# Kernel optimization log

Hardware: AMD Instinct MI355X
Metric: run time of the kernel (lower is better)

The kernel has to match this reference:

```python
import jax, jax.numpy as jnp
import numpy as np

B, N, M, C = 64, 16384, 64, 256
GAMMA = 0.95
EPS = 1e-16


def setup_inputs() -> dict:
    key = jax.random.key(0)
    k0, k1, k2, k3, k4 = jax.random.split(key, 5)
    embeddings = jax.random.normal(k0, (B, C), jnp.float32)
    # previous (w_u, w_r, w_lu) state; normalize so rows look like attention weights
    w_prev = jax.nn.softmax(jax.random.normal(k1, (B, 3, N), jnp.float32), axis=-1)
    memory = jax.random.normal(k2, (B, N, M), jnp.float32) * 0.05
    # fc_write params: xavier_uniform(gain=1.4) weight, N(0, 0.01) bias
    fan_in, fan_out = C, M + 2
    bound = 1.4 * np.sqrt(6.0 / (fan_in + fan_out))
    W = jax.random.uniform(k3, (M + 2, C), jnp.float32, -bound, bound)
    b = jax.random.normal(k4, (M + 2,), jnp.float32) * 0.01
    return {"embeddings": embeddings, "w_prev": w_prev, "memory": memory,
            "W": W, "b": b, "n": 4}


def reference(embeddings, w_prev, memory, W, b, n):
    # fc_write: [B,C] -> [B, M+2], split into key k, strength beta, gate g
    o = embeddings @ W.T + b
    k = o[:, :M]                                   # [B, M]
    beta = jax.nn.softplus(o[:, M:M + 1])          # [B, 1]
    g = jax.nn.sigmoid(o[:, M + 1:M + 2])          # [B, 1]

    w_u_prev = w_prev[:, 0]                        # usage
    w_r_prev = w_prev[:, 1]                        # read
    w_lu_prev = w_prev[:, 2]                       # least-used

    # content addressing: cosine similarity of k against every memory slot
    sim = jnp.einsum('bm,bnm->bn', k, memory) / (
        jnp.linalg.norm(k, axis=-1, keepdims=True)
        * jnp.linalg.norm(memory, axis=-1) + EPS)   # [B, N]
    w_r = jax.nn.softmax(beta * sim, axis=-1)       # [B, N]

    # LRUA write weight: interpolate previous read and least-used weights
    w_w = g * w_r_prev + (1.0 - g) * w_lu_prev      # [B, N]
    # usage decay + accumulate
    w_u = GAMMA * w_u_prev + w_r + w_w              # [B, N]

    # least-used: 1 at the n smallest-usage slots, 0 elsewhere
    _, lu_idx = jax.lax.top_k(-w_u, n)              # [B, n]
    w_lu = jnp.zeros_like(w_u).at[
        jnp.arange(w_u.shape[0])[:, None], lu_idx].set(1.0)

    # lrua_write: rank-1 additive write into memory
    new_memory = memory + w_w[:, :, None] * k[:, None, :]  # [B, N, M]

    w = jnp.stack([w_u, w_r, w_lu], axis=1)         # [B, 3, N]
    return w, new_memory
```

## Files before the change

kernel.cpp:

```cpp
#include <hip/hip_runtime.h>
#include <math.h>

#define Bn 64
#define Nn 16384
#define Mn 64
#define Cn 256
#define MP2 66
#define GAMMA 0.95f
#define EPSF 1e-16f

__global__ __launch_bounds__(128) void k1_proj(
    const float* __restrict__ emb, const float* __restrict__ W,
    const float* __restrict__ bias,
    float* __restrict__ ws_k, float* __restrict__ ws_beta,
    float* __restrict__ ws_g, float* __restrict__ ws_normk) {
  int b = blockIdx.x;
  int tid = threadIdx.x;
  __shared__ float emb_s[Cn];
  __shared__ float k_s[Mn];
  for (int c = tid; c < Cn; c += blockDim.x) emb_s[c] = emb[(size_t)b * Cn + c];
  __syncthreads();
  if (tid < MP2) {
    float sum = bias[tid];
    const float* wrow = W + (size_t)tid * Cn;
    #pragma unroll 4
    for (int c = 0; c < Cn; ++c) sum += emb_s[c] * wrow[c];
    if (tid < Mn) {
      ws_k[(size_t)b * Mn + tid] = sum;
      k_s[tid] = sum;
    } else if (tid == Mn) {
      ws_beta[b] = fmaxf(sum, 0.0f) + log1pf(expf(-fabsf(sum)));
    } else {
      ws_g[b] = 1.0f / (1.0f + expf(-sum));
    }
  }
  __syncthreads();
  if (tid < 64) {
    float v = k_s[tid] * k_s[tid];
    #pragma unroll
    for (int o = 32; o > 0; o >>= 1) v += __shfl_xor(v, o, 64);
    if (tid == 0) ws_normk[b] = sqrtf(v);
  }
}

__global__ __launch_bounds__(256) void k2_main(
    const float* __restrict__ memory, const float* __restrict__ w_prev,
    const float* __restrict__ ws_k, const float* __restrict__ ws_g,
    const float* __restrict__ ws_normk, const float* __restrict__ ws_beta,
    float* __restrict__ p_out, float* __restrict__ new_mem) {
  const int ROWS_PER_BLOCK = 16;
  const int blocks_per_b = Nn / ROWS_PER_BLOCK;
  int b = blockIdx.x / blocks_per_b;
  int n_base = (blockIdx.x % blocks_per_b) * ROWS_PER_BLOCK;
  int tid = threadIdx.x;
  int wave = tid >> 6;
  int lane = tid & 63;
  int row_in_wave = lane >> 4;
  int col4 = lane & 15;
  int n = n_base + wave * 4 + row_in_wave;

  size_t off = ((size_t)b * Nn + n) * Mn + (size_t)col4 * 4;
  const float4 m4 = *(const float4*)(memory + off);
  const float4 k4 = *(const float4*)(ws_k + (size_t)b * Mn + (size_t)col4 * 4);

  float g = ws_g[b];
  float wr_p  = w_prev[((size_t)b * 3 + 1) * Nn + n];
  float wlu_p = w_prev[((size_t)b * 3 + 2) * Nn + n];
  float ww = g * wr_p + (1.0f - g) * wlu_p;

  float dkm = m4.x * k4.x + m4.y * k4.y + m4.z * k4.z + m4.w * k4.w;
  float dmm = m4.x * m4.x + m4.y * m4.y + m4.z * m4.z + m4.w * m4.w;
  #pragma unroll
  for (int o = 8; o >= 1; o >>= 1) {
    dkm += __shfl_xor(dkm, o, 64);
    dmm += __shfl_xor(dmm, o, 64);
  }

  float4 o4;
  o4.x = m4.x + ww * k4.x;
  o4.y = m4.y + ww * k4.y;
  o4.z = m4.z + ww * k4.z;
  o4.w = m4.w + ww * k4.w;
  *(float4*)(new_mem + off) = o4;

  if (col4 == 0) {
    float sim = dkm / (ws_normk[b] * sqrtf(dmm) + EPSF);
    float beta = ws_beta[b];
    p_out[(size_t)b * Nn + n] = expf(beta * (sim - 1.0f));
  }
}

__global__ __launch_bounds__(1024) void k3_finish(
    const float* __restrict__ w_prev, const float* __restrict__ p_in,
    const float* __restrict__ ws_g, float* __restrict__ w_out) {
  int b = blockIdx.x;
  int tid = threadIdx.x;
  int lane = tid & 63, wid = tid >> 6;
  float g = ws_g[b];

  const float* pb     = p_in   + (size_t)b * Nn;
  const float* wup_p  = w_prev + ((size_t)b * 3 + 0) * Nn;
  const float* wrp_p  = w_prev + ((size_t)b * 3 + 1) * Nn;
  const float* wlup_p = w_prev + ((size_t)b * 3 + 2) * Nn;
  float* wu_out  = w_out + ((size_t)b * 3 + 0) * Nn;
  float* wr_out  = w_out + ((size_t)b * 3 + 1) * Nn;
  float* wlu_out = w_out + ((size_t)b * 3 + 2) * Nn;

  float p_loc[16];
  float lsum = 0.0f;
  #pragma unroll
  for (int i = 0; i < 4; ++i) {
    int n0 = i * 4096 + tid * 4;
    float4 p4 = *(const float4*)(pb + n0);
    p_loc[i * 4 + 0] = p4.x;
    p_loc[i * 4 + 1] = p4.y;
    p_loc[i * 4 + 2] = p4.z;
    p_loc[i * 4 + 3] = p4.w;
    lsum += p4.x + p4.y + p4.z + p4.w;
  }
  #pragma unroll
  for (int o = 32; o > 0; o >>= 1) lsum += __shfl_xor(lsum, o, 64);

  __shared__ float red_f[16];
  __shared__ float bcast_f;
  if (lane == 0) red_f[wid] = lsum;
  __syncthreads();
  if (tid == 0) {
    float s = 0.0f;
    for (int i = 0; i < 16; ++i) s += red_f[i];
    bcast_f = s;
  }
  __syncthreads();
  float inv = 1.0f / bcast_f;

  unsigned long long key_loc[16];
  #pragma unroll
  for (int i = 0; i < 4; ++i) {
    int n0 = i * 4096 + tid * 4;
    float4 u4 = *(const float4*)(wup_p + n0);
    float4 r4 = *(const float4*)(wrp_p + n0);
    float4 l4 = *(const float4*)(wlup_p + n0);
    float4 wr4, wu4;
    wr4.x = p_loc[i * 4 + 0] * inv;
    wr4.y = p_loc[i * 4 + 1] * inv;
    wr4.z = p_loc[i * 4 + 2] * inv;
    wr4.w = p_loc[i * 4 + 3] * inv;
    wu4.x = GAMMA * u4.x + wr4.x + (g * r4.x + (1.0f - g) * l4.x);
    wu4.y = GAMMA * u4.y + wr4.y + (g * r4.y + (1.0f - g) * l4.y);
    wu4.z = GAMMA * u4.z + wr4.z + (g * r4.z + (1.0f - g) * l4.z);
    wu4.w = GAMMA * u4.w + wr4.w + (g * r4.w + (1.0f - g) * l4.w);
    *(float4*)(wu_out + n0) = wu4;
    *(float4*)(wr_out + n0) = wr4;
    #pragma unroll
    for (int j = 0; j < 4; ++j) {
      float v = (j == 0) ? wu4.x : (j == 1) ? wu4.y : (j == 2) ? wu4.z : wu4.w;
      unsigned int bits = __float_as_uint(v);
      bits ^= (bits >> 31) ? 0xFFFFFFFFu : 0x80000000u;
      key_loc[i * 4 + j] =
          ((unsigned long long)bits << 32) | (unsigned int)(n0 + j);
    }
  }

  __shared__ unsigned long long red_k[16];
  __shared__ unsigned long long best_s;
  unsigned long long chosen[4] = {~0ull, ~0ull, ~0ull, ~0ull};

  for (int r = 0; r < 4; ++r) {
    unsigned long long bk = ~0ull;
    #pragma unroll
    for (int i = 0; i < 16; ++i) {
      unsigned long long k = key_loc[i];
      bool excl = (k == chosen[0]) | (k == chosen[1]) | (k == chosen[2]) | (k == chosen[3]);
      if (!excl && k < bk) bk = k;
    }
    #pragma unroll
    for (int o = 32; o > 0; o >>= 1) {
      unsigned long long ok = __shfl_xor(bk, o, 64);
      if (ok < bk) bk = ok;
    }
    if (lane == 0) red_k[wid] = bk;
    __syncthreads();
    if (tid == 0) {
      unsigned long long m = red_k[0];
      for (int i = 1; i < 16; ++i) if (red_k[i] < m) m = red_k[i];
      best_s = m;
    }
    __syncthreads();
    chosen[r] = best_s;
  }

  int c0 = (int)(chosen[0] & 0xFFFFFFFFull);
  int c1 = (int)(chosen[1] & 0xFFFFFFFFull);
  int c2 = (int)(chosen[2] & 0xFFFFFFFFull);
  int c3 = (int)(chosen[3] & 0xFFFFFFFFull);

  #pragma unroll
  for (int i = 0; i < 4; ++i) {
    int n0 = i * 4096 + tid * 4;
    float4 v;
    v.x = (n0 + 0 == c0 || n0 + 0 == c1 || n0 + 0 == c2 || n0 + 0 == c3) ? 1.0f : 0.0f;
    v.y = (n0 + 1 == c0 || n0 + 1 == c1 || n0 + 1 == c2 || n0 + 1 == c3) ? 1.0f : 0.0f;
    v.z = (n0 + 2 == c0 || n0 + 2 == c1 || n0 + 2 == c2 || n0 + 2 == c3) ? 1.0f : 0.0f;
    v.w = (n0 + 3 == c0 || n0 + 3 == c1 || n0 + 3 == c2 || n0 + 3 == c3) ? 1.0f : 0.0f;
    *(float4*)(wlu_out + n0) = v;
  }
}

extern "C" void kernel_launch(void* const* d_in, const int* in_sizes, int n_in,
                              void* d_out, int out_size, void* d_ws, size_t ws_size,
                              hipStream_t stream) {
  const float* emb    = (const float*)d_in[0];
  const float* w_prev = (const float*)d_in[1];
  const float* memory = (const float*)d_in[2];
  const float* W      = (const float*)d_in[3];
  const float* bias   = (const float*)d_in[4];

  float* out = (float*)d_out;
  float* w_out   = out;
  float* new_mem = out + (size_t)Bn * 3 * Nn;

  float* ws       = (float*)d_ws;
  float* ws_k     = ws;
  float* ws_beta  = ws_k + (size_t)Bn * Mn;
  float* ws_g     = ws_beta + Bn;
  float* ws_normk = ws_g + Bn;
  float* ws_p     = ws_normk + Bn;

  k1_proj<<<Bn, 128, 0, stream>>>(emb, W, bias, ws_k, ws_beta, ws_g, ws_normk);
  k2_main<<<Bn * (Nn / 16), 256, 0, stream>>>(memory, w_prev, ws_k, ws_g, ws_normk,
                                              ws_beta, ws_p, new_mem);
  k3_finish<<<Bn, 1024, 0, stream>>>(w_prev, ws_p, ws_g, w_out);
}
```

Baseline: 475.9 us.

## Split finish kernel into parallel normalize/local-topk and scatter kernels

The softmax-sum partials are now computed per block in the main kernel, so the finishing stage no longer reduces 16K values itself. The single-block-per-batch finish kernel is replaced by 16 blocks per batch that normalize, write outputs and find a local top-4 of smallest usage, followed by a small kernel that merges the 64 candidates and scatters the ones. This raises parallelism in the tail stage, which previously ran only 64 blocks, at the cost of an extra launch, extra block-level reductions in the main kernel, and each 16-block group re-reading 256 partial sums.

```diff
diff --git a/kernel.cpp b/kernel.cpp
--- a/kernel.cpp
+++ b/kernel.cpp
@@ -8,6 +8,9 @@
 #define MP2 66
 #define GAMMA 0.95f
 #define EPSF 1e-16f
+
+#define K3A_BLKS_PER_B 16
+#define K2_BLKS_PER_B (Nn / 16)
 
 __global__ __launch_bounds__(128) void k1_proj(
     const float* __restrict__ emb, const float* __restrict__ W,
@@ -47,11 +50,11 @@
     const float* __restrict__ memory, const float* __restrict__ w_prev,
     const float* __restrict__ ws_k, const float* __restrict__ ws_g,
     const float* __restrict__ ws_normk, const float* __restrict__ ws_beta,
-    float* __restrict__ p_out, float* __restrict__ new_mem) {
+    float* __restrict__ p_out, float* __restrict__ new_mem,
+    float* __restrict__ ws_psum) {
   const int ROWS_PER_BLOCK = 16;
-  const int blocks_per_b = Nn / ROWS_PER_BLOCK;
-  int b = blockIdx.x / blocks_per_b;
-  int n_base = (blockIdx.x % blocks_per_b) * ROWS_PER_BLOCK;
+  int b = blockIdx.x / K2_BLKS_PER_B;
+  int n_base = (blockIdx.x % K2_BLKS_PER_B) * ROWS_PER_BLOCK;
   int tid = threadIdx.x;
   int wave = tid >> 6;
   int lane = tid & 63;
@@ -83,20 +86,44 @@
   o4.w = m4.w + ww * k4.w;
   *(float4*)(new_mem + off) = o4;
 
-  if (col4 == 0) {
-    float sim = dkm / (ws_normk[b] * sqrtf(dmm) + EPSF);
-    float beta = ws_beta[b];
-    p_out[(size_t)b * Nn + n] = expf(beta * (sim - 1.0f));
-  }
-}
-
-__global__ __launch_bounds__(1024) void k3_finish(
+  float sim = dkm / (ws_normk[b] * sqrtf(dmm) + EPSF);
+  float e = expf(ws_beta[b] * (sim - 1.0f));
+  if (col4 == 0) p_out[(size_t)b * Nn + n] = e;
+
+  __shared__ float esum_s[4];
+  float ec = (col4 == 0) ? e : 0.0f;
+  ec += __shfl_xor(ec, 16, 64);
+  ec += __shfl_xor(ec, 32, 64);
+  if (lane == 0) esum_s[wave] = ec;
+  __syncthreads();
+  if (tid == 0)
+    ws_psum[blockIdx.x] = esum_s[0] + esum_s[1] + esum_s[2] + esum_s[3];
+}
+
+__global__ __launch_bounds__(256) void k3a_norm(
     const float* __restrict__ w_prev, const float* __restrict__ p_in,
-    const float* __restrict__ ws_g, float* __restrict__ w_out) {
-  int b = blockIdx.x;
+    const float* __restrict__ ws_g, const float* __restrict__ ws_psum,
+    float* __restrict__ w_out, unsigned long long* __restrict__ ws_top) {
+  int b = blockIdx.x / K3A_BLKS_PER_B;
+  int blk = blockIdx.x % K3A_BLKS_PER_B;
   int tid = threadIdx.x;
   int lane = tid & 63, wid = tid >> 6;
   float g = ws_g[b];
+
+  __shared__ float red_f[4];
+  __shared__ float bcast_f;
+
+  {
+    float4 s4 = *(const float4*)(ws_psum + (size_t)b * K2_BLKS_PER_B + tid * 4);
+    float s = s4.x + s4.y + s4.z + s4.w;
+    #pragma unroll
+    for (int o = 32; o > 0; o >>= 1) s += __shfl_xor(s, o, 64);
+    if (lane == 0) red_f[wid] = s;
+    __syncthreads();
+    if (tid == 0) bcast_f = red_f[0] + red_f[1] + red_f[2] + red_f[3];
+    __syncthreads();
+  }
+  float inv = 1.0f / bcast_f;
 
   const float* pb     = p_in   + (size_t)b * Nn;
   const float* wup_p  = w_prev + ((size_t)b * 3 + 0) * Nn;
@@ -106,70 +133,41 @@
   float* wr_out  = w_out + ((size_t)b * 3 + 1) * Nn;
   float* wlu_out = w_out + ((size_t)b * 3 + 2) * Nn;
 
-  float p_loc[16];
-  float lsum = 0.0f;
-  #pragma unroll
-  for (int i = 0; i < 4; ++i) {
-    int n0 = i * 4096 + tid * 4;
-    float4 p4 = *(const float4*)(pb + n0);
-    p_loc[i * 4 + 0] = p4.x;
-    p_loc[i * 4 + 1] = p4.y;
-    p_loc[i * 4 + 2] = p4.z;
-    p_loc[i * 4 + 3] = p4.w;
-    lsum += p4.x + p4.y + p4.z + p4.w;
-  }
-  #pragma unroll
-  for (int o = 32; o > 0; o >>= 1) lsum += __shfl_xor(lsum, o, 64);
-
-  __shared__ float red_f[16];
-  __shared__ float bcast_f;
-  if (lane == 0) red_f[wid] = lsum;
-  __syncthreads();
-  if (tid == 0) {
-    float s = 0.0f;
-    for (int i = 0; i < 16; ++i) s += red_f[i];
-    bcast_f = s;
-  }
-  __syncthreads();
-  float inv = 1.0f / bcast_f;
-
-  unsigned long long key_loc[16];
-  #pragma unroll
-  for (int i = 0; i < 4; ++i) {
-    int n0 = i * 4096 + tid * 4;
-    float4 u4 = *(const float4*)(wup_p + n0);
-    float4 r4 = *(const float4*)(wrp_p + n0);
-    float4 l4 = *(const float4*)(wlup_p + n0);
-    float4 wr4, wu4;
-    wr4.x = p_loc[i * 4 + 0] * inv;
-    wr4.y = p_loc[i * 4 + 1] * inv;
-    wr4.z = p_loc[i * 4 + 2] * inv;
-    wr4.w = p_loc[i * 4 + 3] * inv;
-    wu4.x = GAMMA * u4.x + wr4.x + (g * r4.x + (1.0f - g) * l4.x);
-    wu4.y = GAMMA * u4.y + wr4.y + (g * r4.y + (1.0f - g) * l4.y);
-    wu4.z = GAMMA * u4.z + wr4.z + (g * r4.z + (1.0f - g) * l4.z);
-    wu4.w = GAMMA * u4.w + wr4.w + (g * r4.w + (1.0f - g) * l4.w);
-    *(float4*)(wu_out + n0) = wu4;
-    *(float4*)(wr_out + n0) = wr4;
+  int n0 = blk * (Nn / K3A_BLKS_PER_B) + tid * 4;
+  float4 p4 = *(const float4*)(pb + n0);
+  float4 u4 = *(const float4*)(wup_p + n0);
+  float4 r4 = *(const float4*)(wrp_p + n0);
+  float4 l4 = *(const float4*)(wlup_p + n0);
+  float4 wr4, wu4;
+  wr4.x = p4.x * inv; wr4.y = p4.y * inv; wr4.z = p4.z * inv; wr4.w = p4.w * inv;
+  wu4.x = GAMMA * u4.x + wr4.x + (g * r4.x + (1.0f - g) * l4.x);
+  wu4.y = GAMMA * u4.y + wr4.y + (g * r4.y + (1.0f - g) * l4.y);
+  wu4.z = GAMMA * u4.z + wr4.z + (g * r4.z + (1.0f - g) * l4.z);
+  wu4.w = GAMMA * u4.w + wr4.w + (g * r4.w + (1.0f - g) * l4.w);
+  *(float4*)(wu_out + n0) = wu4;
+  *(float4*)(wr_out + n0) = wr4;
+  float4 z4 = make_float4(0.0f, 0.0f, 0.0f, 0.0f);
+  *(float4*)(wlu_out + n0) = z4;
+
+  unsigned long long key[4];
+  {
+    float v[4] = {wu4.x, wu4.y, wu4.z, wu4.w};
     #pragma unroll
     for (int j = 0; j < 4; ++j) {
-      float v = (j == 0) ? wu4.x : (j == 1) ? wu4.y : (j == 2) ? wu4.z : wu4.w;
-      unsigned int bits = __float_as_uint(v);
+      unsigned int bits = __float_as_uint(v[j]);
       bits ^= (bits >> 31) ? 0xFFFFFFFFu : 0x80000000u;
-      key_loc[i * 4 + j] =
-          ((unsigned long long)bits << 32) | (unsigned int)(n0 + j);
-    }
-  }
-
-  __shared__ unsigned long long red_k[16];
-  __shared__ unsigned long long best_s;
+      key[j] = ((unsigned long long)bits << 32) | (unsigned int)(n0 + j);
+    }
+  }
+
+  __shared__ unsigned long long red_k[4];
+  __shared__ unsigned long long chosen_s[4];
   unsigned long long chosen[4] = {~0ull, ~0ull, ~0ull, ~0ull};
-
   for (int r = 0; r < 4; ++r) {
     unsigned long long bk = ~0ull;
     #pragma unroll
-    for (int i = 0; i < 16; ++i) {
-      unsigned long long k = key_loc[i];
+    for (int j = 0; j < 4; ++j) {
+      unsigned long long k = key[j];
       bool excl = (k == chosen[0]) | (k == chosen[1]) | (k == chosen[2]) | (k == chosen[3]);
       if (!excl && k < bk) bk = k;
     }
@@ -182,27 +180,31 @@
     __syncthreads();
     if (tid == 0) {
       unsigned long long m = red_k[0];
-      for (int i = 1; i < 16; ++i) if (red_k[i] < m) m = red_k[i];
-      best_s = m;
-    }
-    __syncthreads();
-    chosen[r] = best_s;
-  }
-
-  int c0 = (int)(chosen[0] & 0xFFFFFFFFull);
-  int c1 = (int)(chosen[1] & 0xFFFFFFFFull);
-  int c2 = (int)(chosen[2] & 0xFFFFFFFFull);
-  int c3 = (int)(chosen[3] & 0xFFFFFFFFull);
-
+      for (int i = 1; i < 4; ++i) if (red_k[i] < m) m = red_k[i];
+      chosen_s[r] = m;
+    }
+    __syncthreads();
+    chosen[r] = chosen_s[r];
+  }
+  if (tid < 4) ws_top[(size_t)blockIdx.x * 4 + tid] = chosen_s[tid];
+}
+
+__global__ __launch_bounds__(64) void k3b_scatter(
+    const unsigned long long* __restrict__ ws_top, float* __restrict__ w_out) {
+  int b = blockIdx.x;
+  int lane = threadIdx.x;
+  unsigned long long k = ws_top[(size_t)b * (K3A_BLKS_PER_B * 4) + lane];
+  float* wlu_out = w_out + ((size_t)b * 3 + 2) * Nn;
   #pragma unroll
-  for (int i = 0; i < 4; ++i) {
-    int n0 = i * 4096 + tid * 4;
-    float4 v;
-    v.x = (n0 + 0 == c0 || n0 + 0 == c1 || n0 + 0 == c2 || n0 + 0 == c3) ? 1.0f : 0.0f;
-    v.y = (n0 + 1 == c0 || n0 + 1 == c1 || n0 + 1 == c2 || n0 + 1 == c3) ? 1.0f : 0.0f;
-    v.z = (n0 + 2 == c0 || n0 + 2 == c1 || n0 + 2 == c2 || n0 + 2 == c3) ? 1.0f : 0.0f;
-    v.w = (n0 + 3 == c0 || n0 + 3 == c1 || n0 + 3 == c2 || n0 + 3 == c3) ? 1.0f : 0.0f;
-    *(float4*)(wlu_out + n0) = v;
+  for (int r = 0; r < 4; ++r) {
+    unsigned long long m = k;
+    #pragma unroll
+    for (int o = 32; o > 0; o >>= 1) {
+      unsigned long long om = __shfl_xor(m, o, 64);
+      if (om < m) m = om;
+    }
+    if (k == m) k = ~0ull;
+    if (lane == r) wlu_out[(unsigned int)(m & 0xFFFFFFFFull)] = 1.0f;
   }
 }
 
@@ -225,9 +227,14 @@
   float* ws_g     = ws_beta + Bn;
   float* ws_normk = ws_g + Bn;
   float* ws_p     = ws_normk + Bn;
+  float* ws_psum  = ws_p + (size_t)Bn * Nn;
+  unsigned long long* ws_top =
+      (unsigned long long*)(ws_psum + (size_t)Bn * K2_BLKS_PER_B);
 
   k1_proj<<<Bn, 128, 0, stream>>>(emb, W, bias, ws_k, ws_beta, ws_g, ws_normk);
-  k2_main<<<Bn * (Nn / 16), 256, 0, stream>>>(memory, w_prev, ws_k, ws_g, ws_normk,
-                                              ws_beta, ws_p, new_mem);
-  k3_finish<<<Bn, 1024, 0, stream>>>(w_prev, ws_p, ws_g, w_out);
-}
+  k2_main<<<Bn * K2_BLKS_PER_B, 256, 0, stream>>>(memory, w_prev, ws_k, ws_g, ws_normk,
+                                                  ws_beta, ws_p, new_mem, ws_psum);
+  k3a_norm<<<Bn * K3A_BLKS_PER_B, 256, 0, stream>>>(w_prev, ws_p, ws_g, ws_psum,
+                                                    w_out, ws_top);
+  k3b_scatter<<<Bn, 64, 0, stream>>>(ws_top, w_out);
+}
```

Result: no change. 474.2 us (-0.4%).
